# Optimization experiments

Measured on AMD Instinct MI355X. Metric: run time of the kernel, lower is better.

## Reference

```python
import jax, jax.numpy as jnp
import numpy as np

D_MODEL = 1536
N_HEADS = 16
HEAD_DIM = D_MODEL // N_HEADS  # 96
NUM_BLOCKS = HEAD_DIM // 24    # 4


def generate_leech_kernel(dim=24):
    base = np.zeros((dim, dim), dtype=np.float32)
    for i in range(dim - 1):
        base[i, i] = 2.0
        base[i, i + 1] = 2.0
    base[-1, -1] = 2.0
    base[-1, 0] = -2.0
    q, _ = np.linalg.qr(base)
    return jnp.asarray(q.astype(np.float32))


def setup_inputs() -> dict:
    key = jax.random.key(0)
    k1, k2, k3 = jax.random.split(key, 3)
    x = jax.random.normal(k1, (2, 2048, D_MODEL), dtype=jnp.float32)
    # nn.Linear weights stored [out, in]; kept that layout, applied as x @ W.T
    w_qkv = jax.random.normal(k2, (3 * D_MODEL, D_MODEL), dtype=jnp.float32) * (D_MODEL ** -0.5)
    w_out = jax.random.normal(k3, (D_MODEL, D_MODEL), dtype=jnp.float32) * (D_MODEL ** -0.5)
    leech_kernel = generate_leech_kernel(24)
    return {"x": x, "w_qkv": w_qkv, "w_out": w_out, "leech_kernel": leech_kernel}


def _apply_kernel(t, kernel):
    # t: [b, h, s, head_dim] -> blockwise 24x24 rotation
    b, h, s, d = t.shape
    t = t.reshape(b, h, s, NUM_BLOCKS, 24)
    t = jnp.einsum('bhsni,ij->bhsnj', t, kernel)
    return t.reshape(b, h, s, d)


def reference(x, w_qkv, w_out, leech_kernel):
    bsz, steps, _ = x.shape
    qkv = x @ w_qkv.T  # [b, s, 3*d]
    qkv = qkv.reshape(bsz, steps, 3, N_HEADS, HEAD_DIM)
    qkv = jnp.transpose(qkv, (2, 0, 3, 1, 4))  # [3, b, h, s, hd]
    q, k, v = qkv[0], qkv[1], qkv[2]
    q = _apply_kernel(q, leech_kernel)
    k = _apply_kernel(k, leech_kernel)
    scale = HEAD_DIM ** -0.5
    scores = jnp.einsum('bhqd,bhkd->bhqk', q, k) * scale
    attn = jax.nn.softmax(scores, axis=-1)
    out = jnp.einsum('bhqk,bhkd->bhqd', attn, v)
    out = jnp.transpose(out, (0, 2, 1, 3)).reshape(bsz, steps, -1)
    return out @ w_out.T
```

## Files before the change

kernel.cpp:

```cpp
#include <hip/hip_runtime.h>
#include <cmath>

#define D_MODEL 1536
#define N_HEADS 16
#define HEAD_DIM 96
#define SEQ 2048
#define BATCH 2
#define M_TOTAL 4096
#define N_QKV 4608
#define QK_LOG2E 0.14724449f

typedef unsigned short ushort_t;
typedef __attribute__((ext_vector_type(8))) short bf16x8;
typedef __attribute__((ext_vector_type(4))) float f32x4;

static __device__ __forceinline__ ushort_t f2bf(float f) {
    unsigned u = __builtin_bit_cast(unsigned, f);
    u += 0x7fffu + ((u >> 16) & 1u);
    return (ushort_t)(u >> 16);
}

static __device__ __forceinline__ unsigned pk2bf(float lo, float hi) {
#if __has_builtin(__builtin_amdgcn_cvt_pk_bf16_f32)
    auto v = __builtin_amdgcn_cvt_pk_bf16_f32(lo, hi);
    return __builtin_bit_cast(unsigned, v);
#else
    return (unsigned)f2bf(lo) | ((unsigned)f2bf(hi) << 16);
#endif
}

static __device__ __forceinline__ float fast_exp2(float x) {
#if __has_builtin(__builtin_amdgcn_exp2f)
    return __builtin_amdgcn_exp2f(x);
#else
    return __expf(x * 0.69314718056f);
#endif
}

typedef const __attribute__((address_space(1))) unsigned int* gas_t;
typedef __attribute__((address_space(3))) unsigned int* las_t;
static __device__ __forceinline__ void gld_lds16(const void* g, void* l) {
    __builtin_amdgcn_global_load_lds((gas_t)g, (las_t)l, 16, 0, 0);
}

#define MFMA16(a, b, c) __builtin_amdgcn_mfma_f32_16x16x32_bf16(a, b, c, 0, 0, 0)

__global__ __launch_bounds__(256) void convert_f32_bf16(
    const float* __restrict__ in, ushort_t* __restrict__ out, int n)
{
    const int i = (blockIdx.x * 256 + threadIdx.x) * 4;
    if (i >= n) return;
    float4 v = *(const float4*)(in + i);
    ushort4 o;
    o.x = f2bf(v.x); o.y = f2bf(v.y); o.z = f2bf(v.z); o.w = f2bf(v.w);
    *(ushort4*)(out + i) = o;
}

__global__ __launch_bounds__(256) void prep_wqkv(
    const float* __restrict__ W, const float* __restrict__ Kern,
    ushort_t* __restrict__ Wb)
{
    __shared__ float Kl[576];
    const int t = threadIdx.x;
    for (int i = t; i < 576; i += 256) Kl[i] = Kern[i];
    __syncthreads();
    const int g = blockIdx.y;
    const int k = blockIdx.x * 256 + t;
    const float* src = W + (size_t)g * 24 * D_MODEL + k;
    ushort_t* dst = Wb + (size_t)g * 24 * D_MODEL + k;
    if (g < 128) {
        float in[24];
#pragma unroll
        for (int i = 0; i < 24; ++i) in[i] = src[(size_t)i * D_MODEL];
#pragma unroll
        for (int j = 0; j < 24; ++j) {
            float s = 0.f;
#pragma unroll
            for (int i = 0; i < 24; ++i) s = fmaf(in[i], Kl[i * 24 + j], s);
            dst[(size_t)j * D_MODEL] = f2bf(s);
        }
    } else {
#pragma unroll
        for (int i = 0; i < 24; ++i) dst[(size_t)i * D_MODEL] = f2bf(src[(size_t)i * D_MODEL]);
    }
}

__global__ __launch_bounds__(256, 3) void gemm_qkv_bf16(
    const ushort_t* __restrict__ X, const ushort_t* __restrict__ W,
    ushort_t* __restrict__ qb, ushort_t* __restrict__ kb, ushort_t* __restrict__ vb)
{
    __shared__ ushort_t As[128 * 32];
    __shared__ ushort_t Bs[128 * 32];
    const int t = threadIdx.x;
    const int lane = t & 63, w = t >> 6;
    const int c = lane & 15, qd = lane >> 4;
    const int m0 = blockIdx.y * 128, n0 = blockIdx.x * 128;
    const int wr = (w >> 1) * 64, wc = (w & 1) * 64;
    const int sr = lane >> 2, sc = (lane & 3) * 16;
    const char* Xb = (const char*)X;
    const char* Wp = (const char*)W;
    const size_t rowb = 2 * D_MODEL;

    f32x4 acc[4][4];
#pragma unroll
    for (int i = 0; i < 4; ++i)
#pragma unroll
        for (int j = 0; j < 4; ++j) acc[i][j] = {0.f, 0.f, 0.f, 0.f};

    for (int k0 = 0; k0 < D_MODEL; k0 += 32) {
        __syncthreads();
#pragma unroll
        for (int j = 0; j < 2; ++j) {
            const int g = w * 2 + j;
            gld_lds16(Xb + (size_t)(m0 + g * 16 + sr) * rowb + k0 * 2 + sc,
                      (char*)As + g * 1024);
            gld_lds16(Wp + (size_t)(n0 + g * 16 + sr) * rowb + k0 * 2 + sc,
                      (char*)Bs + g * 1024);
        }
        __syncthreads();
        bf16x8 af[4], bfr[4];
#pragma unroll
        for (int i = 0; i < 4; ++i)
            af[i] = *(const bf16x8*)&As[(wr + i * 16 + c) * 32 + qd * 8];
#pragma unroll
        for (int j = 0; j < 4; ++j)
            bfr[j] = *(const bf16x8*)&Bs[(wc + j * 16 + c) * 32 + qd * 8];
#pragma unroll
        for (int i = 0; i < 4; ++i)
#pragma unroll
            for (int j = 0; j < 4; ++j)
                acc[i][j] = MFMA16(af[i], bfr[j], acc[i][j]);
    }
#pragma unroll
    for (int j = 0; j < 4; ++j) {
        const int n = n0 + wc + j * 16 + c;
        const int which = n / D_MODEL;
        const int rem = n % D_MODEL;
        const int head = rem / HEAD_DIM;
        const int d = rem % HEAD_DIM;
        ushort_t* dst = which == 0 ? qb : which == 1 ? kb : vb;
        const float sc2 = which == 0 ? QK_LOG2E : 1.0f;
#pragma unroll
        for (int i = 0; i < 4; ++i)
#pragma unroll
            for (int r = 0; r < 4; ++r) {
                const int m = m0 + wr + i * 16 + qd * 4 + r;
                const int b_ = m >> 11, s_ = m & (SEQ - 1);
                dst[((size_t)(b_ * N_HEADS + head) * SEQ + s_) * HEAD_DIM + d] =
                    f2bf(acc[i][j][r] * sc2);
            }
    }
}

__global__ __launch_bounds__(256, 3) void gemm_out_bf16(
    const ushort_t* __restrict__ A, const ushort_t* __restrict__ W,
    float* __restrict__ C)
{
    __shared__ ushort_t As[128 * 32];
    __shared__ ushort_t Bs[128 * 32];
    const int t = threadIdx.x;
    const int lane = t & 63, w = t >> 6;
    const int c = lane & 15, qd = lane >> 4;
    const int m0 = blockIdx.y * 128, n0 = blockIdx.x * 128;
    const int wr = (w >> 1) * 64, wc = (w & 1) * 64;
    const int sr = lane >> 2, sc = (lane & 3) * 16;
    const char* Ab = (const char*)A;
    const char* Wp = (const char*)W;
    const size_t rowb = 2 * D_MODEL;

    f32x4 acc[4][4];
#pragma unroll
    for (int i = 0; i < 4; ++i)
#pragma unroll
        for (int j = 0; j < 4; ++j) acc[i][j] = {0.f, 0.f, 0.f, 0.f};

    for (int k0 = 0; k0 < D_MODEL; k0 += 32) {
        __syncthreads();
#pragma unroll
        for (int j = 0; j < 2; ++j) {
            const int g = w * 2 + j;
            gld_lds16(Ab + (size_t)(m0 + g * 16 + sr) * rowb + k0 * 2 + sc,
                      (char*)As + g * 1024);
            gld_lds16(Wp + (size_t)(n0 + g * 16 + sr) * rowb + k0 * 2 + sc,
                      (char*)Bs + g * 1024);
        }
        __syncthreads();
        bf16x8 af[4], bfr[4];
#pragma unroll
        for (int i = 0; i < 4; ++i)
            af[i] = *(const bf16x8*)&As[(wr + i * 16 + c) * 32 + qd * 8];
#pragma unroll
        for (int j = 0; j < 4; ++j)
            bfr[j] = *(const bf16x8*)&Bs[(wc + j * 16 + c) * 32 + qd * 8];
#pragma unroll
        for (int i = 0; i < 4; ++i)
#pragma unroll
            for (int j = 0; j < 4; ++j)
                acc[i][j] = MFMA16(af[i], bfr[j], acc[i][j]);
    }
#pragma unroll
    for (int i = 0; i < 4; ++i)
#pragma unroll
        for (int j = 0; j < 4; ++j)
#pragma unroll
            for (int r = 0; r < 4; ++r)
                C[(size_t)(m0 + wr + i * 16 + qd * 4 + r) * D_MODEL + n0 + wc + j * 16 + c] =
                    acc[i][j][r];
}

__global__ __launch_bounds__(256, 3) void flash_bf16(
    const ushort_t* __restrict__ Q, const ushort_t* __restrict__ K,
    const ushort_t* __restrict__ V, ushort_t* __restrict__ attn)
{
    __shared__ ushort_t Ks[12 * 64 * 8];
    __shared__ ushort_t Vt[96 * 72];
    __shared__ ushort_t Ps[4][32 * 72];

    const int t = threadIdx.x;
    const int lane = t & 63, w = t >> 6;
    const int c = lane & 15, qd = lane >> 4;
    const int h = blockIdx.y, bb = blockIdx.z;
    const int q0 = blockIdx.x * 128;
    const size_t base = ((size_t)(bb * N_HEADS + h)) * SEQ * HEAD_DIM;
    const ushort_t* Qb = Q + base;
    const char* Kb = (const char*)(K + base);
    const ushort_t* Vb = V + base;

    bf16x8 aq[2][3];
#pragma unroll
    for (int qi = 0; qi < 2; ++qi)
#pragma unroll
        for (int kc = 0; kc < 3; ++kc)
            aq[qi][kc] = *(const bf16x8*)(Qb +
                (size_t)(q0 + w * 32 + qi * 16 + c) * HEAD_DIM + kc * 32 + qd * 8);

    f32x4 oacc[6][2];
#pragma unroll
    for (int jd = 0; jd < 6; ++jd)
#pragma unroll
        for (int qi = 0; qi < 2; ++qi) oacc[jd][qi] = {0.f, 0.f, 0.f, 0.f};
    float lrow[2] = {0.f, 0.f};

    bf16x8 vreg[3];
    {
        const ushort_t* vp = Vb + (size_t)lane * HEAD_DIM + w * 24;
#pragma unroll
        for (int jv = 0; jv < 3; ++jv) vreg[jv] = *(const bf16x8*)(vp + jv * 8);
    }

    for (int kt = 0; kt < SEQ / 64; ++kt) {
        __syncthreads();
        {
            const char* kp = Kb + (size_t)kt * 64 * 192;
#pragma unroll
            for (int jj = 0; jj < 3; ++jj) {
                const int g = w * 3 + jj;
                gld_lds16(kp + (size_t)lane * 192 + g * 16, (char*)Ks + g * 1024);
            }
        }
#pragma unroll
        for (int jv = 0; jv < 3; ++jv)
#pragma unroll
            for (int e = 0; e < 8; ++e)
                Vt[(w * 24 + jv * 8 + e) * 72 + lane] = (ushort_t)vreg[jv][e];
        {
            const int ktn = (kt + 1 < SEQ / 64) ? kt + 1 : kt;
            const ushort_t* vp = Vb + (size_t)(ktn * 64 + lane) * HEAD_DIM + w * 24;
#pragma unroll
            for (int jv = 0; jv < 3; ++jv) vreg[jv] = *(const bf16x8*)(vp + jv * 8);
        }
        __syncthreads();

        f32x4 sacc[4][2];
#pragma unroll
        for (int kti = 0; kti < 4; ++kti)
#pragma unroll
            for (int qi = 0; qi < 2; ++qi) sacc[kti][qi] = {0.f, 0.f, 0.f, 0.f};
#pragma unroll
        for (int kc = 0; kc < 3; ++kc) {
            bf16x8 ak[4];
#pragma unroll
            for (int kti = 0; kti < 4; ++kti)
                ak[kti] = *(const bf16x8*)&Ks[((kc * 4 + qd) * 64 + kti * 16 + c) * 8];
#pragma unroll
            for (int kti = 0; kti < 4; ++kti)
#pragma unroll
                for (int qi = 0; qi < 2; ++qi)
                    sacc[kti][qi] = MFMA16(ak[kti], aq[qi][kc], sacc[kti][qi]);
        }

        float ls0 = 0.f, ls1 = 0.f;
#pragma unroll
        for (int kti = 0; kti < 4; ++kti)
#pragma unroll
            for (int qi = 0; qi < 2; ++qi) {
                const float p0 = fast_exp2(sacc[kti][qi][0]);
                const float p1 = fast_exp2(sacc[kti][qi][1]);
                const float p2 = fast_exp2(sacc[kti][qi][2]);
                const float p3 = fast_exp2(sacc[kti][qi][3]);
                uint2 pk;
                pk.x = pk2bf(p0, p1);
                pk.y = pk2bf(p2, p3);
                *(uint2*)&Ps[w][(qi * 16 + c) * 72 + kti * 16 + qd * 4] = pk;
                const float s = (p0 + p1) + (p2 + p3);
                if (qi == 0) ls0 += s; else ls1 += s;
            }
        ls0 += __shfl_xor(ls0, 16, 64); ls0 += __shfl_xor(ls0, 32, 64);
        ls1 += __shfl_xor(ls1, 16, 64); ls1 += __shfl_xor(ls1, 32, 64);
        lrow[0] += ls0; lrow[1] += ls1;

#pragma unroll
        for (int kc = 0; kc < 2; ++kc) {
            bf16x8 bp[2];
#pragma unroll
            for (int qi = 0; qi < 2; ++qi)
                bp[qi] = *(const bf16x8*)&Ps[w][(qi * 16 + c) * 72 + kc * 32 + qd * 8];
#pragma unroll
            for (int jd = 0; jd < 6; ++jd) {
                const bf16x8 av = *(const bf16x8*)&Vt[(jd * 16 + c) * 72 + kc * 32 + qd * 8];
#pragma unroll
                for (int qi = 0; qi < 2; ++qi)
                    oacc[jd][qi] = MFMA16(av, bp[qi], oacc[jd][qi]);
            }
        }
    }

#pragma unroll
    for (int qi = 0; qi < 2; ++qi) {
        const float linv = 1.0f / lrow[qi];
        const int row = bb * SEQ + q0 + w * 32 + qi * 16 + c;
        ushort_t* dst = attn + (size_t)row * D_MODEL + h * HEAD_DIM + qd * 4;
#pragma unroll
        for (int jd = 0; jd < 6; ++jd) {
            ushort4 o4;
            o4.x = f2bf(oacc[jd][qi][0] * linv);
            o4.y = f2bf(oacc[jd][qi][1] * linv);
            o4.z = f2bf(oacc[jd][qi][2] * linv);
            o4.w = f2bf(oacc[jd][qi][3] * linv);
            *(ushort4*)(dst + jd * 16) = o4;
        }
    }
}


extern "C" void kernel_launch(void* const* d_in, const int* in_sizes, int n_in,
                              void* d_out, int out_size, void* d_ws, size_t ws_size,
                              hipStream_t stream)
{
    const float* x     = (const float*)d_in[0];
    const float* w_qkv = (const float*)d_in[1];
    const float* w_out = (const float*)d_in[2];
    const float* leech = (const float*)d_in[3];
    float* out = (float*)d_out;
    char* ws = (char*)d_ws;

    ushort_t* xb    = (ushort_t*)(ws);
    ushort_t* wqkvb = (ushort_t*)(ws + 12582912);
    ushort_t* woutb = (ushort_t*)(ws + 26738688);
    ushort_t* qb    = (ushort_t*)(ws + 31457280);
    ushort_t* kb    = (ushort_t*)(ws + 44040192);
    ushort_t* vb    = (ushort_t*)(ws + 56623104);
    ushort_t* attnb = (ushort_t*)(ws + 69206016);

    convert_f32_bf16<<<6144, 256, 0, stream>>>(x, xb, M_TOTAL * D_MODEL);
    prep_wqkv<<<dim3(6, 192), 256, 0, stream>>>(w_qkv, leech, wqkvb);
    convert_f32_bf16<<<2304, 256, 0, stream>>>(w_out, woutb, D_MODEL * D_MODEL);

    gemm_qkv_bf16<<<dim3(N_QKV / 128, M_TOTAL / 128), 256, 0, stream>>>(
        xb, wqkvb, qb, kb, vb);

    flash_bf16<<<dim3(SEQ / 128, N_HEADS, BATCH), 256, 0, stream>>>(
        qb, kb, vb, attnb);

    gemm_out_bf16<<<dim3(D_MODEL / 128, M_TOTAL / 128), 256, 0, stream>>>(
        attnb, woutb, out);
}
```

Before: 302.9 us.

## Emit V transposed from QKV GEMM, deepen GEMM K-tile with XOR-swizzled LDS

The QKV GEMM now writes V in a transposed [b,h,d,s] layout, so the flash kernel can load V^T tiles straight into LDS with direct global-to-LDS copies. This replaces the old register staging and scalar per-element transpose stores. Both GEMMs double the K tile to 64 and use an XOR-swizzled LDS layout to avoid bank conflicts, and their launch bounds are raised to 4 blocks per CU. The costs are twice the LDS per GEMM block, which may limit occupancy, and uncoalesced-looking strided 8-byte stores for V^T in the GEMM epilogue.

```diff
diff --git a/kernel.cpp b/kernel.cpp
--- a/kernel.cpp
+++ b/kernel.cpp
@@ -85,18 +85,19 @@
     }
 }
 
-__global__ __launch_bounds__(256, 3) void gemm_qkv_bf16(
+__global__ __launch_bounds__(256, 4) void gemm_qkv_bf16(
     const ushort_t* __restrict__ X, const ushort_t* __restrict__ W,
-    ushort_t* __restrict__ qb, ushort_t* __restrict__ kb, ushort_t* __restrict__ vb)
-{
-    __shared__ ushort_t As[128 * 32];
-    __shared__ ushort_t Bs[128 * 32];
+    ushort_t* __restrict__ qb, ushort_t* __restrict__ kb, ushort_t* __restrict__ vtb)
+{
+    __shared__ ushort_t As[128 * 64];
+    __shared__ ushort_t Bs[128 * 64];
     const int t = threadIdx.x;
     const int lane = t & 63, w = t >> 6;
     const int c = lane & 15, qd = lane >> 4;
     const int m0 = blockIdx.y * 128, n0 = blockIdx.x * 128;
     const int wr = (w >> 1) * 64, wc = (w & 1) * 64;
-    const int sr = lane >> 2, sc = (lane & 3) * 16;
+    const int lr = lane >> 3;
+    const int lc = (lane & 7) ^ lr;
     const char* Xb = (const char*)X;
     const char* Wp = (const char*)W;
     const size_t rowb = 2 * D_MODEL;
@@ -107,29 +108,34 @@
 #pragma unroll
         for (int j = 0; j < 4; ++j) acc[i][j] = {0.f, 0.f, 0.f, 0.f};
 
-    for (int k0 = 0; k0 < D_MODEL; k0 += 32) {
-        __syncthreads();
-#pragma unroll
-        for (int j = 0; j < 2; ++j) {
-            const int g = w * 2 + j;
-            gld_lds16(Xb + (size_t)(m0 + g * 16 + sr) * rowb + k0 * 2 + sc,
+    for (int k0 = 0; k0 < D_MODEL; k0 += 64) {
+        __syncthreads();
+#pragma unroll
+        for (int j = 0; j < 4; ++j) {
+            const int g = w * 4 + j;
+            const int row = g * 8 + lr;
+            gld_lds16(Xb + (size_t)(m0 + row) * rowb + k0 * 2 + lc * 16,
                       (char*)As + g * 1024);
-            gld_lds16(Wp + (size_t)(n0 + g * 16 + sr) * rowb + k0 * 2 + sc,
+            gld_lds16(Wp + (size_t)(n0 + row) * rowb + k0 * 2 + lc * 16,
                       (char*)Bs + g * 1024);
         }
         __syncthreads();
-        bf16x8 af[4], bfr[4];
-#pragma unroll
-        for (int i = 0; i < 4; ++i)
-            af[i] = *(const bf16x8*)&As[(wr + i * 16 + c) * 32 + qd * 8];
-#pragma unroll
-        for (int j = 0; j < 4; ++j)
-            bfr[j] = *(const bf16x8*)&Bs[(wc + j * 16 + c) * 32 + qd * 8];
-#pragma unroll
-        for (int i = 0; i < 4; ++i)
+#pragma unroll
+        for (int kc = 0; kc < 2; ++kc) {
+            const int sx = ((kc * 4 + qd) ^ (c & 7)) * 16;
+            bf16x8 af[4], bfr[4];
+#pragma unroll
+            for (int i = 0; i < 4; ++i)
+                af[i] = *(const bf16x8*)((const char*)As + (wr + i * 16 + c) * 128 + sx);
 #pragma unroll
             for (int j = 0; j < 4; ++j)
-                acc[i][j] = MFMA16(af[i], bfr[j], acc[i][j]);
+                bfr[j] = *(const bf16x8*)((const char*)Bs + (wc + j * 16 + c) * 128 + sx);
+#pragma unroll
+            for (int i = 0; i < 4; ++i)
+#pragma unroll
+                for (int j = 0; j < 4; ++j)
+                    acc[i][j] = MFMA16(af[i], bfr[j], acc[i][j]);
+        }
     }
 #pragma unroll
     for (int j = 0; j < 4; ++j) {
@@ -138,32 +144,46 @@
         const int rem = n % D_MODEL;
         const int head = rem / HEAD_DIM;
         const int d = rem % HEAD_DIM;
-        ushort_t* dst = which == 0 ? qb : which == 1 ? kb : vb;
-        const float sc2 = which == 0 ? QK_LOG2E : 1.0f;
-#pragma unroll
-        for (int i = 0; i < 4; ++i)
-#pragma unroll
-            for (int r = 0; r < 4; ++r) {
-                const int m = m0 + wr + i * 16 + qd * 4 + r;
-                const int b_ = m >> 11, s_ = m & (SEQ - 1);
-                dst[((size_t)(b_ * N_HEADS + head) * SEQ + s_) * HEAD_DIM + d] =
-                    f2bf(acc[i][j][r] * sc2);
+        if (which < 2) {
+            ushort_t* dst = which == 0 ? qb : kb;
+            const float sc2 = which == 0 ? QK_LOG2E : 1.0f;
+#pragma unroll
+            for (int i = 0; i < 4; ++i)
+#pragma unroll
+                for (int r = 0; r < 4; ++r) {
+                    const int m = m0 + wr + i * 16 + qd * 4 + r;
+                    const int b_ = m >> 11, s_ = m & (SEQ - 1);
+                    dst[((size_t)(b_ * N_HEADS + head) * SEQ + s_) * HEAD_DIM + d] =
+                        f2bf(acc[i][j][r] * sc2);
+                }
+        } else {
+            const int b_ = m0 >> 11;
+            const int sb = (m0 & (SEQ - 1)) + wr + qd * 4;
+            ushort_t* dstv = vtb + ((size_t)(b_ * N_HEADS + head) * HEAD_DIM + d) * SEQ;
+#pragma unroll
+            for (int i = 0; i < 4; ++i) {
+                ushort4 o4;
+                o4.x = f2bf(acc[i][j][0]); o4.y = f2bf(acc[i][j][1]);
+                o4.z = f2bf(acc[i][j][2]); o4.w = f2bf(acc[i][j][3]);
+                *(ushort4*)&dstv[sb + i * 16] = o4;
             }
-    }
-}
-
-__global__ __launch_bounds__(256, 3) void gemm_out_bf16(
+        }
+    }
+}
+
+__global__ __launch_bounds__(256, 4) void gemm_out_bf16(
     const ushort_t* __restrict__ A, const ushort_t* __restrict__ W,
     float* __restrict__ C)
 {
-    __shared__ ushort_t As[128 * 32];
-    __shared__ ushort_t Bs[128 * 32];
+    __shared__ ushort_t As[128 * 64];
+    __shared__ ushort_t Bs[128 * 64];
     const int t = threadIdx.x;
     const int lane = t & 63, w = t >> 6;
     const int c = lane & 15, qd = lane >> 4;
     const int m0 = blockIdx.y * 128, n0 = blockIdx.x * 128;
     const int wr = (w >> 1) * 64, wc = (w & 1) * 64;
-    const int sr = lane >> 2, sc = (lane & 3) * 16;
+    const int lr = lane >> 3;
+    const int lc = (lane & 7) ^ lr;
     const char* Ab = (const char*)A;
     const char* Wp = (const char*)W;
     const size_t rowb = 2 * D_MODEL;
@@ -174,29 +194,34 @@
 #pragma unroll
         for (int j = 0; j < 4; ++j) acc[i][j] = {0.f, 0.f, 0.f, 0.f};
 
-    for (int k0 = 0; k0 < D_MODEL; k0 += 32) {
-        __syncthreads();
-#pragma unroll
-        for (int j = 0; j < 2; ++j) {
-            const int g = w * 2 + j;
-            gld_lds16(Ab + (size_t)(m0 + g * 16 + sr) * rowb + k0 * 2 + sc,
+    for (int k0 = 0; k0 < D_MODEL; k0 += 64) {
+        __syncthreads();
+#pragma unroll
+        for (int j = 0; j < 4; ++j) {
+            const int g = w * 4 + j;
+            const int row = g * 8 + lr;
+            gld_lds16(Ab + (size_t)(m0 + row) * rowb + k0 * 2 + lc * 16,
                       (char*)As + g * 1024);
-            gld_lds16(Wp + (size_t)(n0 + g * 16 + sr) * rowb + k0 * 2 + sc,
+            gld_lds16(Wp + (size_t)(n0 + row) * rowb + k0 * 2 + lc * 16,
                       (char*)Bs + g * 1024);
         }
         __syncthreads();
-        bf16x8 af[4], bfr[4];
-#pragma unroll
-        for (int i = 0; i < 4; ++i)
-            af[i] = *(const bf16x8*)&As[(wr + i * 16 + c) * 32 + qd * 8];
-#pragma unroll
-        for (int j = 0; j < 4; ++j)
-            bfr[j] = *(const bf16x8*)&Bs[(wc + j * 16 + c) * 32 + qd * 8];
-#pragma unroll
-        for (int i = 0; i < 4; ++i)
+#pragma unroll
+        for (int kc = 0; kc < 2; ++kc) {
+            const int sx = ((kc * 4 + qd) ^ (c & 7)) * 16;
+            bf16x8 af[4], bfr[4];
+#pragma unroll
+            for (int i = 0; i < 4; ++i)
+                af[i] = *(const bf16x8*)((const char*)As + (wr + i * 16 + c) * 128 + sx);
 #pragma unroll
             for (int j = 0; j < 4; ++j)
-                acc[i][j] = MFMA16(af[i], bfr[j], acc[i][j]);
+                bfr[j] = *(const bf16x8*)((const char*)Bs + (wc + j * 16 + c) * 128 + sx);
+#pragma unroll
+            for (int i = 0; i < 4; ++i)
+#pragma unroll
+                for (int j = 0; j < 4; ++j)
+                    acc[i][j] = MFMA16(af[i], bfr[j], acc[i][j]);
+        }
     }
 #pragma unroll
     for (int i = 0; i < 4; ++i)
@@ -210,21 +235,23 @@
 
 __global__ __launch_bounds__(256, 3) void flash_bf16(
     const ushort_t* __restrict__ Q, const ushort_t* __restrict__ K,
-    const ushort_t* __restrict__ V, ushort_t* __restrict__ attn)
+    const ushort_t* __restrict__ VT, ushort_t* __restrict__ attn)
 {
     __shared__ ushort_t Ks[12 * 64 * 8];
-    __shared__ ushort_t Vt[96 * 72];
+    __shared__ ushort_t Vt[96 * 64];
     __shared__ ushort_t Ps[4][32 * 72];
 
     const int t = threadIdx.x;
     const int lane = t & 63, w = t >> 6;
     const int c = lane & 15, qd = lane >> 4;
+    const int lr = lane >> 3;
+    const int lc = (lane & 7) ^ lr;
     const int h = blockIdx.y, bb = blockIdx.z;
     const int q0 = blockIdx.x * 128;
     const size_t base = ((size_t)(bb * N_HEADS + h)) * SEQ * HEAD_DIM;
     const ushort_t* Qb = Q + base;
     const char* Kb = (const char*)(K + base);
-    const ushort_t* Vb = V + base;
+    const ushort_t* VTb = VT + base;
 
     bf16x8 aq[2][3];
 #pragma unroll
@@ -240,13 +267,6 @@
 #pragma unroll
         for (int qi = 0; qi < 2; ++qi) oacc[jd][qi] = {0.f, 0.f, 0.f, 0.f};
     float lrow[2] = {0.f, 0.f};
-
-    bf16x8 vreg[3];
-    {
-        const ushort_t* vp = Vb + (size_t)lane * HEAD_DIM + w * 24;
-#pragma unroll
-        for (int jv = 0; jv < 3; ++jv) vreg[jv] = *(const bf16x8*)(vp + jv * 8);
-    }
 
     for (int kt = 0; kt < SEQ / 64; ++kt) {
         __syncthreads();
@@ -259,15 +279,11 @@
             }
         }
 #pragma unroll
-        for (int jv = 0; jv < 3; ++jv)
-#pragma unroll
-            for (int e = 0; e < 8; ++e)
-                Vt[(w * 24 + jv * 8 + e) * 72 + lane] = (ushort_t)vreg[jv][e];
-        {
-            const int ktn = (kt + 1 < SEQ / 64) ? kt + 1 : kt;
-            const ushort_t* vp = Vb + (size_t)(ktn * 64 + lane) * HEAD_DIM + w * 24;
-#pragma unroll
-            for (int jv = 0; jv < 3; ++jv) vreg[jv] = *(const bf16x8*)(vp + jv * 8);
+        for (int jj = 0; jj < 3; ++jj) {
+            const int g = w * 3 + jj;
+            const int d = g * 8 + lr;
+            gld_lds16((const char*)(VTb + (size_t)d * SEQ + kt * 64 + lc * 8),
+                      (char*)Vt + g * 1024);
         }
         __syncthreads();
 
@@ -317,7 +333,9 @@
                 bp[qi] = *(const bf16x8*)&Ps[w][(qi * 16 + c) * 72 + kc * 32 + qd * 8];
 #pragma unroll
             for (int jd = 0; jd < 6; ++jd) {
-                const bf16x8 av = *(const bf16x8*)&Vt[(jd * 16 + c) * 72 + kc * 32 + qd * 8];
+                const int sx = ((kc * 4 + qd) ^ (c & 7)) * 16;
+                const bf16x8 av =
+                    *(const bf16x8*)((const char*)Vt + (jd * 16 + c) * 128 + sx);
 #pragma unroll
                 for (int qi = 0; qi < 2; ++qi)
                     oacc[jd][qi] = MFMA16(av, bp[qi], oacc[jd][qi]);
@@ -359,7 +377,7 @@
     ushort_t* woutb = (ushort_t*)(ws + 26738688);
     ushort_t* qb    = (ushort_t*)(ws + 31457280);
     ushort_t* kb    = (ushort_t*)(ws + 44040192);
-    ushort_t* vb    = (ushort_t*)(ws + 56623104);
+    ushort_t* vtb   = (ushort_t*)(ws + 56623104);
     ushort_t* attnb = (ushort_t*)(ws + 69206016);
 
     convert_f32_bf16<<<6144, 256, 0, stream>>>(x, xb, M_TOTAL * D_MODEL);
@@ -367,10 +385,10 @@
     convert_f32_bf16<<<2304, 256, 0, stream>>>(w_out, woutb, D_MODEL * D_MODEL);
 
     gemm_qkv_bf16<<<dim3(N_QKV / 128, M_TOTAL / 128), 256, 0, stream>>>(
-        xb, wqkvb, qb, kb, vb);
+        xb, wqkvb, qb, kb, vtb);
 
     flash_bf16<<<dim3(SEQ / 128, N_HEADS, BATCH), 256, 0, stream>>>(
-        qb, kb, vb, attnb);
+        qb, kb, vtb, attnb);
 
     gemm_out_bf16<<<dim3(D_MODEL / 128, M_TOTAL / 128), 256, 0, stream>>>(
         attnb, woutb, out);
```

Result: faster. 282.8 us (-6.6%).
